# Kernel tuning notes

Hardware: AMD Instinct MI355X
Metric: run time of the kernel (lower is better)

## Reference

```python
import jax, jax.numpy as jnp
import numpy as np

D = 1024      # d_model
H = 16        # n_head
DH = D // H   # d_head = 64
DFF = 4 * D   # 4096
B, T = 1, 4096
EPS = 1e-5


def _layernorm(x, scale, bias):
    mu = jnp.mean(x, axis=-1, keepdims=True)
    var = jnp.mean(jnp.square(x - mu), axis=-1, keepdims=True)
    return (x - mu) * jax.lax.rsqrt(var + EPS) * scale + bias


def setup_inputs() -> dict:
    key = jax.random.key(0)
    ks = jax.random.split(key, 8)
    s = 0.02
    return {
        "x": jax.random.normal(ks[0], (B, T, D), jnp.float32),
        "ln1_scale": jnp.ones((D,), jnp.float32),
        "ln1_bias": jnp.zeros((D,), jnp.float32),
        "W_attn": jax.random.normal(ks[1], (D, 3 * D), jnp.float32) * s,
        "b_attn": jnp.zeros((3 * D,), jnp.float32),
        "W_proj": jax.random.normal(ks[2], (D, D), jnp.float32) * s,
        "b_proj": jnp.zeros((D,), jnp.float32),
        "ln2_scale": jnp.ones((D,), jnp.float32),
        "ln2_bias": jnp.zeros((D,), jnp.float32),
        "W_fc": jax.random.normal(ks[3], (D, DFF), jnp.float32) * s,
        "b_fc": jnp.zeros((DFF,), jnp.float32),
        "W_fc2": jax.random.normal(ks[4], (DFF, D), jnp.float32) * s,
        "b_fc2": jnp.zeros((D,), jnp.float32),
    }


def reference(x, ln1_scale, ln1_bias, W_attn, b_attn, W_proj, b_proj,
              ln2_scale, ln2_bias, W_fc, b_fc, W_fc2, b_fc2):
    Bx, Tx, C = x.shape
    # --- attention branch ---
    h = _layernorm(x, ln1_scale, ln1_bias)
    qkv = h @ W_attn + b_attn                      # [B,T,3D]
    q, k, v = jnp.split(qkv, 3, axis=-1)
    q = q.reshape(Bx, Tx, H, DH).transpose(0, 2, 1, 3)  # [B,H,T,dh]
    k = k.reshape(Bx, Tx, H, DH).transpose(0, 2, 1, 3)
    v = v.reshape(Bx, Tx, H, DH).transpose(0, 2, 1, 3)
    att = jnp.einsum('bhqd,bhkd->bhqk', q, k) * (1.0 / jnp.sqrt(DH))
    causal = jnp.tril(jnp.ones((Tx, Tx), dtype=jnp.bool_))[None, None]
    att = jnp.where(causal, att, -jnp.inf)
    att = jax.nn.softmax(att, axis=-1)
    y = jnp.einsum('bhqk,bhkd->bhqd', att, v)      # [B,H,T,dh]
    y = y.transpose(0, 2, 1, 3).reshape(Bx, Tx, C)
    y = y @ W_proj + b_proj
    x = x + y
    # --- MLP branch ---
    h2 = _layernorm(x, ln2_scale, ln2_bias)
    m = jax.nn.gelu(h2 @ W_fc + b_fc)              # approximate gelu (flax default)
    m = m @ W_fc2 + b_fc2
    return x + m
```

## Files before the change

kernel.cpp:

```cpp
#include <hip/hip_runtime.h>
#include <hip/hip_bf16.h>

typedef short bf16x8 __attribute__((ext_vector_type(8)));
typedef float f32x4 __attribute__((ext_vector_type(4)));
typedef unsigned short u16;
typedef unsigned int u32;

#define TSEQ 4096
#define DMODEL 1024
#define NHEAD 16
#define DHEAD 64
#define DFF 4096

__device__ __forceinline__ u16 f2bf(float f) {
    u32 u = __builtin_bit_cast(u32, f);
    u32 lsb = (u >> 16) & 1u;
    u += 0x7fffu + lsb;
    return (u16)(u >> 16);
}

__device__ __forceinline__ float exp2_hw(float x) {
    float r;
    asm("v_exp_f32 %0, %1" : "=v"(r) : "v"(x));
    return r;
}

__device__ __forceinline__ float rcp_hw(float x) {
    float r;
    asm("v_rcp_f32 %0, %1" : "=v"(r) : "v"(x));
    return r;
}

__device__ __forceinline__ u32 cvt_pk_bf16(float a, float b) {
    u32 r;
    asm("v_cvt_pk_bf16_f32 %0, %1, %2" : "=v"(r) : "v"(a), "v"(b));
    return r;
}

__device__ __forceinline__ void gload_lds16(const u16* g, u16* l) {
    __builtin_amdgcn_global_load_lds(
        (const __attribute__((address_space(1))) u32*)g,
        (__attribute__((address_space(3))) u32*)l, 16, 0, 0);
}

__global__ __launch_bounds__(256)
void transpose_cast_kernel(const float* __restrict__ W, u16* __restrict__ Wt, int K, int N)
{
    __shared__ float tile[64][65];
    const int t = threadIdx.x;
    const int c = t & 63, r4 = t >> 6;
    const int col0 = blockIdx.x * 64;
    const int row0 = blockIdx.y * 64;
#pragma unroll
    for (int p = 0; p < 16; p++) {
        const int r = 4 * p + r4;
        tile[r][c] = W[(size_t)(row0 + r) * N + col0 + c];
    }
    __syncthreads();
#pragma unroll
    for (int p = 0; p < 16; p++) {
        const int r = 4 * p + r4;
        Wt[(size_t)(col0 + r) * K + row0 + c] = f2bf(tile[c][r]);
    }
}

__global__ __launch_bounds__(256)
void v_transpose_kernel(const u16* __restrict__ qkv, u16* __restrict__ Vtg)
{
    __shared__ u16 tile[64][72];
    const int t = threadIdx.x;
    const int hh = blockIdx.y, t0 = blockIdx.x * 64;
#pragma unroll
    for (int p = 0; p < 2; p++) {
        const int L = p * 2048 + t * 8;
        const int r = L >> 6, c = L & 63;
        const bf16x8 v = *(const bf16x8*)(qkv + (size_t)(t0 + r) * 3072 + 2048 + hh * 64 + c);
#pragma unroll
        for (int i = 0; i < 8; i++) tile[c + i][r] = (u16)v[i];
    }
    __syncthreads();
#pragma unroll
    for (int p = 0; p < 2; p++) {
        const int L = p * 2048 + t * 8;
        const int d = L >> 6, c = L & 63;
        bf16x8 v;
#pragma unroll
        for (int i = 0; i < 8; i++) v[i] = (short)tile[d][c + i];
        *(bf16x8*)(Vtg + (size_t)(hh * 64 + d) * TSEQ + t0 + c) = v;
    }
}

__global__ __launch_bounds__(256)
void ln_kernel(const float* __restrict__ x, const float* __restrict__ sc,
               const float* __restrict__ bi, u16* __restrict__ out)
{
    const int lane = threadIdx.x & 63;
    const int row = blockIdx.x * 4 + (threadIdx.x >> 6);
    const float* xr = x + (size_t)row * DMODEL;
    float4 v[4];
    float s = 0.f, s2 = 0.f;
#pragma unroll
    for (int q = 0; q < 4; q++) {
        v[q] = *(const float4*)(xr + 4 * (lane + 64 * q));
        s  += v[q].x + v[q].y + v[q].z + v[q].w;
        s2 += v[q].x * v[q].x + v[q].y * v[q].y + v[q].z * v[q].z + v[q].w * v[q].w;
    }
#pragma unroll
    for (int off = 1; off < 64; off <<= 1) {
        s  += __shfl_xor(s, off);
        s2 += __shfl_xor(s2, off);
    }
    const float mu = s * (1.f / DMODEL);
    const float rstd = rsqrtf(s2 * (1.f / DMODEL) - mu * mu + 1e-5f);
#pragma unroll
    for (int q = 0; q < 4; q++) {
        const int c = 4 * (lane + 64 * q);
        const float4 scv = *(const float4*)(sc + c);
        const float4 biv = *(const float4*)(bi + c);
        ushort4 ov;
        ov.x = f2bf((v[q].x - mu) * rstd * scv.x + biv.x);
        ov.y = f2bf((v[q].y - mu) * rstd * scv.y + biv.y);
        ov.z = f2bf((v[q].z - mu) * rstd * scv.z + biv.z);
        ov.w = f2bf((v[q].w - mu) * rstd * scv.w + biv.w);
        *(ushort4*)(out + (size_t)row * DMODEL + c) = ov;
    }
}

template<int BN, int GELU_F, int OUT_BF16, int HAS_RES, int HAS_BIAS, int FUSE_Z1 = 0>
__global__ __launch_bounds__(256)
void gemm_kernel(const u16* __restrict__ A, int lda,
                 const u16* __restrict__ Bt, int ldb,
                 const float* __restrict__ bias, const float* __restrict__ res,
                 u16* __restrict__ outb, float* __restrict__ outf0,
                 float* __restrict__ outf1, int M, int N, int Kblk)
{
    constexpr int MI = (BN == 128) ? 4 : 2;
    __shared__ u16 Alds[128 * 64];
    __shared__ u16 Blds[BN * 64];
    const int t = threadIdx.x;
    const int lane = t & 63, w = t >> 6;
    const int g = lane >> 4, fr = lane & 15;
    const int m0 = blockIdx.y * 128, n0 = blockIdx.x * BN;
    const size_t koff = (size_t)blockIdx.z * Kblk;
    const int rowbase = (BN == 128) ? (w >> 1) * 64 : w * 32;
    const int colbase = (BN == 128) ? (w & 1) * 64 : 0;
    float* outf = blockIdx.z ? outf1 : outf0;

    f32x4 zero4 = {0.f, 0.f, 0.f, 0.f};
    f32x4 acc[MI][4];
#pragma unroll
    for (int i = 0; i < MI; i++)
#pragma unroll
        for (int j = 0; j < 4; j++) acc[i][j] = zero4;

    for (int k0 = 0; k0 < Kblk; k0 += 64) {
        __syncthreads();
#pragma unroll
        for (int p = 0; p < 4; p++) {
            const int c = p * 256 + t;
            const int r = c >> 3, j = (c & 7) ^ (r & 7);
            gload_lds16(A + (size_t)(m0 + r) * lda + koff + k0 + j * 8, Alds + c * 8);
        }
#pragma unroll
        for (int p = 0; p < (BN == 128 ? 4 : 2); p++) {
            const int c = p * 256 + t;
            const int r = c >> 3, j = (c & 7) ^ (r & 7);
            gload_lds16(Bt + (size_t)(n0 + r) * ldb + koff + k0 + j * 8, Blds + c * 8);
        }
        __syncthreads();

#pragma unroll
        for (int ks = 0; ks < 2; ks++) {
            bf16x8 af[MI], bfr[4];
#pragma unroll
            for (int i = 0; i < MI; i++)
                af[i] = *(const bf16x8*)(Alds + (rowbase + i * 16 + fr) * 64 + (((ks * 4 + g) ^ (fr & 7)) * 8));
#pragma unroll
            for (int j = 0; j < 4; j++)
                bfr[j] = *(const bf16x8*)(Blds + (colbase + j * 16 + fr) * 64 + (((ks * 4 + g) ^ (fr & 7)) * 8));
#pragma unroll
            for (int i = 0; i < MI; i++)
#pragma unroll
                for (int j = 0; j < 4; j++)
                    acc[i][j] = __builtin_amdgcn_mfma_f32_16x16x32_bf16(af[i], bfr[j], acc[i][j], 0, 0, 0);
        }
    }

    const bool fuse = FUSE_Z1 && (blockIdx.z == 1);
#pragma unroll
    for (int j = 0; j < 4; j++) {
        const int col = n0 + colbase + j * 16 + fr;
        float bv = 0.f;
        if (HAS_BIAS) bv = bias[col];
        if (FUSE_Z1 && fuse) bv = bias[col];
#pragma unroll
        for (int i = 0; i < MI; i++) {
#pragma unroll
            for (int r = 0; r < 4; r++) {
                const int row = m0 + rowbase + i * 16 + g * 4 + r;
                float v = acc[i][j][r] + bv;
                if (GELU_F) {
                    const float q = 0.7978845608028654f * (v + 0.044715f * v * v * v);
                    const float e = exp2_hw(fminf(q, 30.f) * 2.8853900817779268f);
                    v = v * e * rcp_hw(e + 1.0f);
                }
                if (HAS_RES) v += res[(size_t)row * N + col];
                if (FUSE_Z1 && fuse) v += res[(size_t)row * N + col];
                if (OUT_BF16) outb[(size_t)row * N + col] = f2bf(v);
                else          outf[(size_t)row * N + col] = v;
            }
        }
    }
}

__global__ __launch_bounds__(256)
void fc2_merge_kernel(float* __restrict__ out, const float* __restrict__ part)
{
    const int i = blockIdx.x * 256 + threadIdx.x;
    const float4 o = ((const float4*)out)[i];
    const float4 p = ((const float4*)part)[i];
    float4 v;
    v.x = o.x + p.x;
    v.y = o.y + p.y;
    v.z = o.z + p.z;
    v.w = o.w + p.w;
    ((float4*)out)[i] = v;
}

__device__ __forceinline__ void softmax_update(
    const f32x4 st[4], bool diag, int klim, int g, int fr,
    float& mrow, float& lrow, f32x4 o[4], u16* Pl)
{
    const float ninf = -__builtin_inff();
    const float C = 0.125f * 1.4426950408889634f;
    float av[4][4];
#pragma unroll
    for (int ct = 0; ct < 4; ct++)
#pragma unroll
        for (int r = 0; r < 4; r++) {
            float aa = st[ct][r];
            if (diag && (ct * 16 + g * 4 + r) > klim) aa = ninf;
            av[ct][r] = aa;
        }
    float m0 = fmaxf(fmaxf(av[0][0], av[0][1]), fmaxf(av[0][2], av[0][3]));
    float m1 = fmaxf(fmaxf(av[1][0], av[1][1]), fmaxf(av[1][2], av[1][3]));
    float m2 = fmaxf(fmaxf(av[2][0], av[2][1]), fmaxf(av[2][2], av[2][3]));
    float m3 = fmaxf(fmaxf(av[3][0], av[3][1]), fmaxf(av[3][2], av[3][3]));
    float vm = fmaxf(fmaxf(m0, m1), fmaxf(m2, m3));
    vm = fmaxf(vm, __shfl_xor(vm, 16));
    vm = fmaxf(vm, __shfl_xor(vm, 32));
    const float mn = (vm <= mrow + 64.f) ? mrow : vm;
    const float mnC = mn * C;
    float rs = 0.f;
#pragma unroll
    for (int ct = 0; ct < 4; ct++) {
        const float p0 = exp2_hw(__builtin_fmaf(av[ct][0], C, -mnC));
        const float p1 = exp2_hw(__builtin_fmaf(av[ct][1], C, -mnC));
        const float p2 = exp2_hw(__builtin_fmaf(av[ct][2], C, -mnC));
        const float p3 = exp2_hw(__builtin_fmaf(av[ct][3], C, -mnC));
        rs += (p0 + p1) + (p2 + p3);
        uint2 pk;
        pk.x = cvt_pk_bf16(p0, p1);
        pk.y = cvt_pk_bf16(p2, p3);
        const int chunk = ct * 2 + (g >> 1);
        const int addr = fr * 64 + ((chunk ^ (fr & 7)) * 8) + (g & 1) * 4;
        *(uint2*)(Pl + addr) = pk;
    }
    rs += __shfl_xor(rs, 16);
    rs += __shfl_xor(rs, 32);
    const float sc = exp2_hw((mrow - mn) * C);
    lrow = __builtin_fmaf(lrow, sc, rs);
    const bool nores = (mn == mrow);
    mrow = mn;
    if (!__all(nores)) {
        float scb[4];
#pragma unroll
        for (int j = 0; j < 4; j++) scb[j] = __shfl(sc, g * 4 + j);
#pragma unroll
        for (int dt = 0; dt < 4; dt++)
#pragma unroll
            for (int j = 0; j < 4; j++) o[dt][j] *= scb[j];
    }
}

__global__ __launch_bounds__(512, 4)
void attn_kernel(const u16* __restrict__ qkv, const u16* __restrict__ Vtg,
                 u16* __restrict__ y)
{
    __shared__ __align__(16) u16 SMEM[24576];
    u16* Klds = SMEM;
    u16* Vlds = SMEM + 128 * 64;
    u16* Pbase = SMEM + 2 * 128 * 64;
    const int t = threadIdx.x, lane = t & 63, w = t >> 6;
    const int g = lane >> 4, fr = lane & 15;
    const int wv = w & 3, grp = w >> 2;
    u16* Pl = Pbase + w * (16 * 64);
    const int hh = blockIdx.y;
    const int ii = blockIdx.x;
    const int ntB = 64 - ii;
    const int qAw = ii * 64 + wv * 16;
    const int qBw = (63 - ii) * 64 + wv * 16;

    bf16x8 aqA[2], aqB[2];
#pragma unroll
    for (int s = 0; s < 2; s++) {
        aqA[s] = *(const bf16x8*)(qkv + (size_t)(qAw + fr) * 3072 + hh * 64 + s * 32 + g * 8);
        aqB[s] = *(const bf16x8*)(qkv + (size_t)(qBw + fr) * 3072 + hh * 64 + s * 32 + g * 8);
    }

    f32x4 zero4 = {0.f, 0.f, 0.f, 0.f};
    f32x4 oA[4] = {zero4, zero4, zero4, zero4};
    f32x4 oB[4] = {zero4, zero4, zero4, zero4};
    const float ninf = -__builtin_inff();
    float mA = ninf, lA = 0.f, mB = ninf, lB = 0.f;

    const int cK0 = t, cK1 = t + 512;
    const int rK0 = cK0 >> 3, jK0 = (cK0 & 7) ^ (rK0 & 7);
    const int rK1 = cK1 >> 3, jK1 = (cK1 & 7) ^ (rK1 & 7);
    const int rv0 = cK0 >> 4, cj0 = cK0 & 15;
    const int jv0 = (cj0 & 8) | ((cj0 & 7) ^ (rv0 & 7));
    const int rv1 = cK1 >> 4, cj1 = cK1 & 15;
    const int jv1 = (cj1 & 8) | ((cj1 & 7) ^ (rv1 & 7));
    const u16* gk0 = qkv + (size_t)rK0 * 3072 + 1024 + hh * 64 + jK0 * 8;
    const u16* gk1 = qkv + (size_t)rK1 * 3072 + 1024 + hh * 64 + jK1 * 8;
    const u16* gv0 = Vtg + (size_t)(hh * 64 + rv0) * TSEQ + jv0 * 8;
    const u16* gv1 = Vtg + (size_t)(hh * 64 + rv1) * TSEQ + jv1 * 8;

    const int nIter = (65 - ii) >> 1;
    for (int j = 0; j < nIter; j++) {
        const int k0 = j * 128;
        __syncthreads();
        gload_lds16(gk0 + (size_t)k0 * 3072, Klds + cK0 * 8);
        gload_lds16(gk1 + (size_t)k0 * 3072, Klds + cK1 * 8);
        gload_lds16(gv0 + k0, Vlds + cK0 * 8);
        gload_lds16(gv1 + k0, Vlds + cK1 * 8);
        __syncthreads();

        const int kt = 2 * j + grp;
        const bool aB = kt < ntB;
        const bool aA = kt <= ii;
        if (aB | aA) {
            const u16* Kl = Klds + grp * (64 * 64);
            const u16* Vl = Vlds;
            const int klim = wv * 16 + fr;

            f32x4 stA[4] = {zero4, zero4, zero4, zero4};
            f32x4 stB[4] = {zero4, zero4, zero4, zero4};
#pragma unroll
            for (int ct = 0; ct < 4; ct++) {
#pragma unroll
                for (int ds = 0; ds < 2; ds++) {
                    const bf16x8 bk = *(const bf16x8*)(Kl + (ct * 16 + fr) * 64 + (((ds * 4 + g) ^ (fr & 7)) * 8));
                    if (aB) stB[ct] = __builtin_amdgcn_mfma_f32_16x16x32_bf16(bk, aqB[ds], stB[ct], 0, 0, 0);
                    if (aA) stA[ct] = __builtin_amdgcn_mfma_f32_16x16x32_bf16(bk, aqA[ds], stA[ct], 0, 0, 0);
                }
            }

            if (aB) {
                softmax_update(stB, kt == ntB - 1, klim, g, fr, mB, lB, oB, Pl);
                __builtin_amdgcn_s_waitcnt(0xc07f);
#pragma unroll
                for (int kkh = 0; kkh < 2; kkh++) {
                    const bf16x8 pa = *(const bf16x8*)(Pl + fr * 64 + (((kkh * 4 + g) ^ (fr & 7)) * 8));
#pragma unroll
                    for (int dt = 0; dt < 4; dt++) {
                        const int cc = grp * 8 + kkh * 4 + g;
                        const bf16x8 bv = *(const bf16x8*)(Vl + (dt * 16 + fr) * 128 + (((cc & 8) | ((cc & 7) ^ (fr & 7))) * 8));
                        oB[dt] = __builtin_amdgcn_mfma_f32_16x16x32_bf16(pa, bv, oB[dt], 0, 0, 0);
                    }
                }
            }
            if (aA) {
                softmax_update(stA, kt == ii, klim, g, fr, mA, lA, oA, Pl);
                __builtin_amdgcn_s_waitcnt(0xc07f);
#pragma unroll
                for (int kkh = 0; kkh < 2; kkh++) {
                    const bf16x8 pa = *(const bf16x8*)(Pl + fr * 64 + (((kkh * 4 + g) ^ (fr & 7)) * 8));
#pragma unroll
                    for (int dt = 0; dt < 4; dt++) {
                        const int cc = grp * 8 + kkh * 4 + g;
                        const bf16x8 bv = *(const bf16x8*)(Vl + (dt * 16 + fr) * 128 + (((cc & 8) | ((cc & 7) ^ (fr & 7))) * 8));
                        oA[dt] = __builtin_amdgcn_mfma_f32_16x16x32_bf16(pa, bv, oA[dt], 0, 0, 0);
                    }
                }
            }
        }
    }

    __syncthreads();
    float* Of = (float*)SMEM;
    float2* Ml = (float2*)Pbase;
    const float C = 0.125f * 1.4426950408889634f;
    if (grp == 1) {
#pragma unroll
        for (int dt = 0; dt < 4; dt++)
#pragma unroll
            for (int jq = 0; jq < 4; jq++) {
                Of[((wv * 2 + 0) * 16 + g * 4 + jq) * 64 + dt * 16 + fr] = oA[dt][jq];
                Of[((wv * 2 + 1) * 16 + g * 4 + jq) * 64 + dt * 16 + fr] = oB[dt][jq];
            }
        if (g == 0) {
            Ml[(wv * 2 + 0) * 16 + fr] = make_float2(mA, lA);
            Ml[(wv * 2 + 1) * 16 + fr] = make_float2(mB, lB);
        }
    }
    __syncthreads();
    if (grp == 0) {
#pragma unroll
        for (int jq = 0; jq < 4; jq++) {
            {
                const float m0 = __shfl(mA, g * 4 + jq), l0 = __shfl(lA, g * 4 + jq);
                const float2 ml1 = Ml[(wv * 2 + 0) * 16 + g * 4 + jq];
                const float mm = fmaxf(m0, ml1.x);
                const float s0 = exp2_hw((m0 - mm) * C);
                const float s1 = exp2_hw((ml1.x - mm) * C);
                const float rl = rcp_hw(__builtin_fmaf(l0, s0, ml1.y * s1));
#pragma unroll
                for (int dt = 0; dt < 4; dt++) {
                    const float o1 = Of[((wv * 2 + 0) * 16 + g * 4 + jq) * 64 + dt * 16 + fr];
                    y[(size_t)(qAw + g * 4 + jq) * DMODEL + hh * 64 + dt * 16 + fr] =
                        f2bf((oA[dt][jq] * s0 + o1 * s1) * rl);
                }
            }
            {
                const float m0 = __shfl(mB, g * 4 + jq), l0 = __shfl(lB, g * 4 + jq);
                const float2 ml1 = Ml[(wv * 2 + 1) * 16 + g * 4 + jq];
                const float mm = fmaxf(m0, ml1.x);
                const float s0 = exp2_hw((m0 - mm) * C);
                const float s1 = exp2_hw((ml1.x - mm) * C);
                const float rl = rcp_hw(__builtin_fmaf(l0, s0, ml1.y * s1));
#pragma unroll
                for (int dt = 0; dt < 4; dt++) {
                    const float o1 = Of[((wv * 2 + 1) * 16 + g * 4 + jq) * 64 + dt * 16 + fr];
                    y[(size_t)(qBw + g * 4 + jq) * DMODEL + hh * 64 + dt * 16 + fr] =
                        f2bf((oB[dt][jq] * s0 + o1 * s1) * rl);
                }
            }
        }
    }
}

extern "C" void kernel_launch(void* const* d_in, const int* in_sizes, int n_in,
                              void* d_out, int out_size, void* d_ws, size_t ws_size,
                              hipStream_t stream)
{
    const float* x      = (const float*)d_in[0];
    const float* ln1_s  = (const float*)d_in[1];
    const float* ln1_b  = (const float*)d_in[2];
    const float* W_attn = (const float*)d_in[3];
    const float* b_attn = (const float*)d_in[4];
    const float* W_proj = (const float*)d_in[5];
    const float* b_proj = (const float*)d_in[6];
    const float* ln2_s  = (const float*)d_in[7];
    const float* ln2_b  = (const float*)d_in[8];
    const float* W_fc   = (const float*)d_in[9];
    const float* b_fc   = (const float*)d_in[10];
    const float* W_fc2  = (const float*)d_in[11];
    const float* b_fc2  = (const float*)d_in[12];
    float* out = (float*)d_out;

    char* ws = (char*)d_ws;
    u16* WtAttn = (u16*)ws; ws += (size_t)3072 * 1024 * 2;
    u16* WtProj = (u16*)ws; ws += (size_t)1024 * 1024 * 2;
    u16* WtFc   = (u16*)ws; ws += (size_t)4096 * 1024 * 2;
    u16* WtFc2  = (u16*)ws; ws += (size_t)1024 * 4096 * 2;
    u16* bufA   = (u16*)ws; ws += (size_t)4096 * 1024 * 2;
    u16* bufB   = (u16*)ws; ws += (size_t)4096 * 4096 * 2;
    float* x1   = (float*)ws; ws += (size_t)4096 * 1024 * 4;
    u16* Vtg    = (u16*)x1;
    float* P0   = (float*)d_ws;

    transpose_cast_kernel<<<dim3(3072 / 64, 1024 / 64), 256, 0, stream>>>(W_attn, WtAttn, 1024, 3072);
    transpose_cast_kernel<<<dim3(1024 / 64, 1024 / 64), 256, 0, stream>>>(W_proj, WtProj, 1024, 1024);
    transpose_cast_kernel<<<dim3(4096 / 64, 1024 / 64), 256, 0, stream>>>(W_fc,   WtFc,   1024, 4096);
    transpose_cast_kernel<<<dim3(1024 / 64, 4096 / 64), 256, 0, stream>>>(W_fc2,  WtFc2,  4096, 1024);

    ln_kernel<<<TSEQ / 4, 256, 0, stream>>>(x, ln1_s, ln1_b, bufA);
    gemm_kernel<128, 0, 1, 0, 1><<<dim3(24, 32, 1), 256, 0, stream>>>(
        bufA, 1024, WtAttn, 1024, b_attn, nullptr, bufB, nullptr, nullptr, 4096, 3072, 1024);
    v_transpose_kernel<<<dim3(TSEQ / 64, NHEAD), 256, 0, stream>>>(bufB, Vtg);
    attn_kernel<<<dim3(32, NHEAD), 512, 0, stream>>>(bufB, Vtg, bufA);
    gemm_kernel<64, 0, 0, 1, 1><<<dim3(16, 32, 1), 256, 0, stream>>>(
        bufA, 1024, WtProj, 1024, b_proj, x, nullptr, x1, nullptr, 4096, 1024, 1024);

    ln_kernel<<<TSEQ / 4, 256, 0, stream>>>(x1, ln2_s, ln2_b, bufA);
    gemm_kernel<128, 1, 1, 0, 1><<<dim3(32, 32, 1), 256, 0, stream>>>(
        bufA, 1024, WtFc, 1024, b_fc, nullptr, bufB, nullptr, nullptr, 4096, 4096, 1024);
    gemm_kernel<128, 0, 0, 0, 0, 1><<<dim3(8, 32, 2), 256, 0, stream>>>(
        bufB, 4096, WtFc2, 4096, b_fc2, x1, nullptr, P0, out, 4096, 1024, 2048);
    fc2_merge_kernel<<<4096, 256, 0, stream>>>(out, P0);
}
```

Baseline: 300.3 us.

## Split attention KV loop across three wave groups with 192-key tiles

Attention blocks grow from 8 to 12 waves, so three wave groups each process a 64-key slice of a 192-key K/V tile per iteration instead of two groups over 128 keys. This cuts the number of loop iterations and barriers and shares each staged tile across more waves. The epilogue now merges three partial softmax states through shared memory. The cost is more LDS per block, lower launch-bound occupancy, and idle groups on the ragged final tile.

```diff
diff --git a/kernel.cpp b/kernel.cpp
--- a/kernel.cpp
+++ b/kernel.cpp
@@ -283,14 +283,14 @@
     }
 }
 
-__global__ __launch_bounds__(512, 4)
+__global__ __launch_bounds__(768, 2)
 void attn_kernel(const u16* __restrict__ qkv, const u16* __restrict__ Vtg,
                  u16* __restrict__ y)
 {
-    __shared__ __align__(16) u16 SMEM[24576];
+    __shared__ __align__(16) u16 SMEM[36864];
     u16* Klds = SMEM;
-    u16* Vlds = SMEM + 128 * 64;
-    u16* Pbase = SMEM + 2 * 128 * 64;
+    u16* Vlds = SMEM + 192 * 64;
+    u16* Pbase = SMEM + 2 * 192 * 64;
     const int t = threadIdx.x, lane = t & 63, w = t >> 6;
     const int g = lane >> 4, fr = lane & 15;
     const int wv = w & 3, grp = w >> 2;
@@ -314,21 +314,21 @@
     const float ninf = -__builtin_inff();
     float mA = ninf, lA = 0.f, mB = ninf, lB = 0.f;
 
-    const int cK0 = t, cK1 = t + 512;
+    const int cK0 = t, cK1 = t + 768;
     const int rK0 = cK0 >> 3, jK0 = (cK0 & 7) ^ (rK0 & 7);
     const int rK1 = cK1 >> 3, jK1 = (cK1 & 7) ^ (rK1 & 7);
-    const int rv0 = cK0 >> 4, cj0 = cK0 & 15;
-    const int jv0 = (cj0 & 8) | ((cj0 & 7) ^ (rv0 & 7));
-    const int rv1 = cK1 >> 4, cj1 = cK1 & 15;
-    const int jv1 = (cj1 & 8) | ((cj1 & 7) ^ (rv1 & 7));
+    const int rv0 = cK0 / 24, cj0 = cK0 - rv0 * 24;
+    const int jv0 = (cj0 & 24) | ((cj0 & 7) ^ (rv0 & 7));
+    const int rv1 = cK1 / 24, cj1 = cK1 - rv1 * 24;
+    const int jv1 = (cj1 & 24) | ((cj1 & 7) ^ (rv1 & 7));
     const u16* gk0 = qkv + (size_t)rK0 * 3072 + 1024 + hh * 64 + jK0 * 8;
     const u16* gk1 = qkv + (size_t)rK1 * 3072 + 1024 + hh * 64 + jK1 * 8;
     const u16* gv0 = Vtg + (size_t)(hh * 64 + rv0) * TSEQ + jv0 * 8;
     const u16* gv1 = Vtg + (size_t)(hh * 64 + rv1) * TSEQ + jv1 * 8;
 
-    const int nIter = (65 - ii) >> 1;
+    const int nIter = (66 - ii) / 3;
     for (int j = 0; j < nIter; j++) {
-        const int k0 = j * 128;
+        const int k0 = j * 192;
         __syncthreads();
         gload_lds16(gk0 + (size_t)k0 * 3072, Klds + cK0 * 8);
         gload_lds16(gk1 + (size_t)k0 * 3072, Klds + cK1 * 8);
@@ -336,12 +336,11 @@
         gload_lds16(gv1 + k0, Vlds + cK1 * 8);
         __syncthreads();
 
-        const int kt = 2 * j + grp;
+        const int kt = 3 * j + grp;
         const bool aB = kt < ntB;
         const bool aA = kt <= ii;
         if (aB | aA) {
             const u16* Kl = Klds + grp * (64 * 64);
-            const u16* Vl = Vlds;
             const int klim = wv * 16 + fr;
 
             f32x4 stA[4] = {zero4, zero4, zero4, zero4};
@@ -365,7 +364,7 @@
 #pragma unroll
                     for (int dt = 0; dt < 4; dt++) {
                         const int cc = grp * 8 + kkh * 4 + g;
-                        const bf16x8 bv = *(const bf16x8*)(Vl + (dt * 16 + fr) * 128 + (((cc & 8) | ((cc & 7) ^ (fr & 7))) * 8));
+                        const bf16x8 bv = *(const bf16x8*)(Vlds + (dt * 16 + fr) * 192 + (((cc & 24) | ((cc & 7) ^ (fr & 7))) * 8));
                         oB[dt] = __builtin_amdgcn_mfma_f32_16x16x32_bf16(pa, bv, oB[dt], 0, 0, 0);
                     }
                 }
@@ -379,7 +378,7 @@
 #pragma unroll
                     for (int dt = 0; dt < 4; dt++) {
                         const int cc = grp * 8 + kkh * 4 + g;
-                        const bf16x8 bv = *(const bf16x8*)(Vl + (dt * 16 + fr) * 128 + (((cc & 8) | ((cc & 7) ^ (fr & 7))) * 8));
+                        const bf16x8 bv = *(const bf16x8*)(Vlds + (dt * 16 + fr) * 192 + (((cc & 24) | ((cc & 7) ^ (fr & 7))) * 8));
                         oA[dt] = __builtin_amdgcn_mfma_f32_16x16x32_bf16(pa, bv, oA[dt], 0, 0, 0);
                     }
                 }
@@ -389,51 +388,47 @@
 
     __syncthreads();
     float* Of = (float*)SMEM;
-    float2* Ml = (float2*)Pbase;
+    float2* Ml = (float2*)(SMEM + 32768);
     const float C = 0.125f * 1.4426950408889634f;
-    if (grp == 1) {
+    if (grp >= 1) {
+        const int gb = (grp - 1) * 8192;
 #pragma unroll
         for (int dt = 0; dt < 4; dt++)
 #pragma unroll
             for (int jq = 0; jq < 4; jq++) {
-                Of[((wv * 2 + 0) * 16 + g * 4 + jq) * 64 + dt * 16 + fr] = oA[dt][jq];
-                Of[((wv * 2 + 1) * 16 + g * 4 + jq) * 64 + dt * 16 + fr] = oB[dt][jq];
+                Of[gb + ((wv * 2 + 0) * 16 + g * 4 + jq) * 64 + dt * 16 + fr] = oA[dt][jq];
+                Of[gb + ((wv * 2 + 1) * 16 + g * 4 + jq) * 64 + dt * 16 + fr] = oB[dt][jq];
             }
         if (g == 0) {
-            Ml[(wv * 2 + 0) * 16 + fr] = make_float2(mA, lA);
-            Ml[(wv * 2 + 1) * 16 + fr] = make_float2(mB, lB);
+            Ml[(grp - 1) * 128 + (wv * 2 + 0) * 16 + fr] = make_float2(mA, lA);
+            Ml[(grp - 1) * 128 + (wv * 2 + 1) * 16 + fr] = make_float2(mB, lB);
         }
     }
     __syncthreads();
     if (grp == 0) {
 #pragma unroll
-        for (int jq = 0; jq < 4; jq++) {
-            {
-                const float m0 = __shfl(mA, g * 4 + jq), l0 = __shfl(lA, g * 4 + jq);
-                const float2 ml1 = Ml[(wv * 2 + 0) * 16 + g * 4 + jq];
-                const float mm = fmaxf(m0, ml1.x);
+        for (int s = 0; s < 2; s++) {
+            const float mown = s ? mB : mA;
+            const float lown = s ? lB : lA;
+            const f32x4* oown = s ? oB : oA;
+            const int qw = s ? qBw : qAw;
+#pragma unroll
+            for (int jq = 0; jq < 4; jq++) {
+                const float m0 = __shfl(mown, g * 4 + jq), l0 = __shfl(lown, g * 4 + jq);
+                const float2 ml1 = Ml[0 * 128 + (wv * 2 + s) * 16 + g * 4 + jq];
+                const float2 ml2 = Ml[1 * 128 + (wv * 2 + s) * 16 + g * 4 + jq];
+                const float mm = fmaxf(fmaxf(m0, ml1.x), ml2.x);
                 const float s0 = exp2_hw((m0 - mm) * C);
                 const float s1 = exp2_hw((ml1.x - mm) * C);
-                const float rl = rcp_hw(__builtin_fmaf(l0, s0, ml1.y * s1));
+                const float s2 = exp2_hw((ml2.x - mm) * C);
+                const float rl = rcp_hw(l0 * s0 + ml1.y * s1 + ml2.y * s2);
+                const int ob = ((wv * 2 + s) * 16 + g * 4 + jq) * 64;
 #pragma unroll
                 for (int dt = 0; dt < 4; dt++) {
-                    const float o1 = Of[((wv * 2 + 0) * 16 + g * 4 + jq) * 64 + dt * 16 + fr];
-                    y[(size_t)(qAw + g * 4 + jq) * DMODEL + hh * 64 + dt * 16 + fr] =
-                        f2bf((oA[dt][jq] * s0 + o1 * s1) * rl);
-                }
-            }
-            {
-                const float m0 = __shfl(mB, g * 4 + jq), l0 = __shfl(lB, g * 4 + jq);
-                const float2 ml1 = Ml[(wv * 2 + 1) * 16 + g * 4 + jq];
-                const float mm = fmaxf(m0, ml1.x);
-                const float s0 = exp2_hw((m0 - mm) * C);
-                const float s1 = exp2_hw((ml1.x - mm) * C);
-                const float rl = rcp_hw(__builtin_fmaf(l0, s0, ml1.y * s1));
-#pragma unroll
-                for (int dt = 0; dt < 4; dt++) {
-                    const float o1 = Of[((wv * 2 + 1) * 16 + g * 4 + jq) * 64 + dt * 16 + fr];
-                    y[(size_t)(qBw + g * 4 + jq) * DMODEL + hh * 64 + dt * 16 + fr] =
-                        f2bf((oB[dt][jq] * s0 + o1 * s1) * rl);
+                    const float o1 = Of[ob + dt * 16 + fr];
+                    const float o2 = Of[8192 + ob + dt * 16 + fr];
+                    y[(size_t)(qw + g * 4 + jq) * DMODEL + hh * 64 + dt * 16 + fr] =
+                        f2bf((oown[dt][jq] * s0 + o1 * s1 + o2 * s2) * rl);
                 }
             }
         }
@@ -479,7 +474,7 @@
     gemm_kernel<128, 0, 1, 0, 1><<<dim3(24, 32, 1), 256, 0, stream>>>(
         bufA, 1024, WtAttn, 1024, b_attn, nullptr, bufB, nullptr, nullptr, 4096, 3072, 1024);
     v_transpose_kernel<<<dim3(TSEQ / 64, NHEAD), 256, 0, stream>>>(bufB, Vtg);
-    attn_kernel<<<dim3(32, NHEAD), 512, 0, stream>>>(bufB, Vtg, bufA);
+    attn_kernel<<<dim3(32, NHEAD), 768, 0, stream>>>(bufB, Vtg, bufA);
     gemm_kernel<64, 0, 0, 1, 1><<<dim3(16, 32, 1), 256, 0, stream>>>(
         bufA, 1024, WtProj, 1024, b_proj, x, nullptr, x1, nullptr, 4096, 1024, 1024);
 
```

Result: slower. 338.2 us (+12.6%).
